# Kernel tuning notes

Hardware: AMD Instinct MI355X
Metric: run time of the kernel (lower is better)

Reference implementation:

```python
import jax, jax.numpy as jnp
import numpy as np

B, TQ, TK, D, R, H = 4, 2048, 2048, 1024, 64, 512
TAU_BASE, ASTRO_DECAY = 1.0, 0.95


def setup_inputs() -> dict:
    key = jax.random.key(0)
    ks = jax.random.split(key, 20)
    xav = lambda k, din, dout: jax.random.uniform(k, (din, dout), jnp.float32, -1.0, 1.0) * np.sqrt(6.0 / (din + dout))
    inp = {
        'q_in': jax.random.normal(ks[0], (B, TQ, D), jnp.float32),
        'k_in': jax.random.normal(ks[1], (B, TK, D), jnp.float32),
        'v_in': jax.random.normal(ks[2], (B, TK, D), jnp.float32),
        'astrocyte_state': jnp.zeros((B,), jnp.float32),
        'Wq': xav(ks[3], D, D), 'bq': jnp.zeros((D,), jnp.float32),
        'Wk': xav(ks[4], D, D), 'bk': jnp.zeros((D,), jnp.float32),
        'Wv': xav(ks[5], D, D), 'bv': jnp.zeros((D,), jnp.float32),
        'Wo': xav(ks[6], D, D), 'bo': jnp.zeros((D,), jnp.float32),
        # orthonormal role rows (R <= D): QR of a random D x R matrix, rows = Q^T
        'role_matrix': jnp.linalg.qr(jax.random.normal(ks[7], (D, R), jnp.float32))[0].T,
        'Wr1': xav(ks[8], D, H), 'br1': jnp.zeros((H,), jnp.float32),
        'Wr2': xav(ks[9], H, R),
        'astro_scale': jnp.ones((1,), jnp.float32),
    }
    return inp


def _l2norm(x, axis=-1, eps=1e-12):
    return x / jnp.clip(jnp.linalg.norm(x, axis=axis, keepdims=True), eps)


def _bind_vectors(a, b):
    # holographic (circular-convolution) binding via FFT along feature dim
    n = a.shape[-1]
    return jnp.fft.irfft(jnp.fft.rfft(a, axis=-1) * jnp.fft.rfft(b, axis=-1), n=n, axis=-1)


def _compute_surprise(Q):
    # per-token surprise: RMS-normalized L2 magnitude of projected queries -> (B, T_q)
    return jnp.linalg.norm(Q, axis=-1) / np.sqrt(Q.shape[-1])


def reference(q_in, k_in, v_in, astrocyte_state, Wq, bq, Wk, bk, Wv, bv, Wo, bo,
              role_matrix, Wr1, br1, Wr2, astro_scale):
    Q = q_in @ Wq + bq                      # (B,TQ,D)
    K = k_in @ Wk + bk                      # (B,TK,D)
    V = v_in @ Wv + bv                      # (B,TK,D)

    role_mat_norm = _l2norm(role_matrix)    # (R,D)
    role_logits = jax.nn.relu(K @ Wr1 + br1) @ Wr2          # (B,TK,R)
    role_weights = jax.nn.softmax(role_logits, axis=-1)
    role_vecs = role_weights @ role_mat_norm                 # (B,TK,D)
    K_bound = _bind_vectors(K, role_vecs)                    # (B,TK,D)

    surprise = _compute_surprise(Q)                          # (B,TQ)
    mean_surprise = surprise.mean(axis=-1)                   # (B,)
    new_state = ASTRO_DECAY * astrocyte_state + (1.0 - ASTRO_DECAY) * mean_surprise
    tau_eff = TAU_BASE * jnp.clip(1.0 + astro_scale * new_state, 0.001)[:, None, None]

    q_n = _l2norm(Q)
    k_n = _l2norm(K_bound)
    cos_sim = jnp.einsum('bqd,bkd->bqk', q_n, k_n)           # (B,TQ,TK)
    x = (cos_sim + 1.0) * 0.5
    scores = jnp.clip(1.0 - tau_eff * (1.0 - x) ** 2, 0.0)   # Epanechnikov kernel
    attn = scores / jnp.clip(scores.sum(axis=-1, keepdims=True), 1e-9)
    context = jnp.einsum('bqk,bkd->bqd', attn, V)
    output = context @ Wo + bo
    return output, new_state
```

## Files before the change

kernel.cpp:

```cpp
#include <hip/hip_runtime.h>
#include <stdint.h>


#define Bq 4
#define Tq 2048
#define Dd 1024
#define NT 8192
#define Hh 512
#define Rr_ 64
#define FQ 1024

typedef unsigned short ushort_t;
typedef short s16x8 __attribute__((ext_vector_type(8)));
typedef float floatx4 __attribute__((ext_vector_type(4)));

__device__ __forceinline__ float b2f(ushort_t s) {
  unsigned u = (unsigned)s << 16;
  return __builtin_bit_cast(float, u);
}
__device__ __forceinline__ ushort_t f2b(float f) {
  unsigned u = __builtin_bit_cast(unsigned, f);
  unsigned r = (u + 0x7fffu + ((u >> 16) & 1u)) >> 16;
  return (ushort_t)r;
}

__device__ __forceinline__ void load_lds16(const void* g, void* l) {
  __builtin_amdgcn_global_load_lds((__attribute__((address_space(1))) void*)(g),
                                   (__attribute__((address_space(3))) void*)(l),
                                   16, 0, 0);
}

__global__ __launch_bounds__(512, 2) void gemm256(
    const ushort_t* __restrict__ A, const ushort_t* __restrict__ Bt,
    float* __restrict__ C, ushort_t* __restrict__ Cbf,
    const float* __restrict__ bias_col, const float* __restrict__ bias_row,
    const float* __restrict__ rmul, int rmulStride,
    const float* __restrict__ cmul, int cmulStride,
    const float* __restrict__ tau,
    float* __restrict__ rowsum, int rsStride, int rsMode,
    int K, int lda, int ldb, int ldc,
    long long sA, long long sB, long long sC, int flags)
{
  __shared__ __align__(16) ushort_t lds[2][2][2][256][32];

  const int bz   = blockIdx.z;
  const ushort_t* Ab = A + (size_t)bz * sA;
  const ushort_t* Bb = Bt + (size_t)bz * sB;
  const int tm   = blockIdx.y * 256;
  const int tn   = blockIdx.x * 256;
  const int tid  = threadIdx.x;
  const int wave = tid >> 6;
  const int lane = tid & 63;
  const int wm   = wave >> 2;
  const int wn   = wave & 3;

  const int s_r  = lane >> 2;
  const int s_cg = (((lane & 3) - (s_r >> 1)) & 3);
  const int f_r  = lane & 15;
  const int f_p  = ((((lane >> 4) + (f_r >> 1)) & 3) << 3);

  const int NTILES = K >> 6;

  floatx4 acc[8][4] = {};

#define STAGE256(tt, g, sl)                                                     \
  do {                                                                          \
    const int mat_ = (g) & 1, h_ = (g) >> 1;                                    \
    const ushort_t* src_ = mat_ ? Bb : Ab;                                      \
    const int ld_ = mat_ ? ldb : lda;                                           \
    const int tb_ = mat_ ? tn : tm;                                             \
    const int kofs_ = (tt) * 64 + h_ * 32 + s_cg * 8;                           \
    _Pragma("unroll")                                                           \
    for (int j_ = 0; j_ < 2; j_++) {                                            \
      const int slab_ = wave * 2 + j_;                                          \
      const ushort_t* gp_ = src_ + (size_t)(tb_ + slab_ * 16 + s_r) * ld_ + kofs_; \
      load_lds16(gp_, (void*)&lds[sl][mat_][h_][slab_ * 16][0]);                \
    }                                                                           \
  } while (0)

  STAGE256(0, 0, 0);
  STAGE256(0, 1, 0);
  STAGE256(0, 2, 0);
  STAGE256(0, 3, 0);
  asm volatile("s_waitcnt vmcnt(4)" ::: "memory");
  __builtin_amdgcn_s_barrier();

  for (int t = 0; t < NTILES; t++) {
    const int sl  = t & 1;
    const int sl1 = sl ^ 1;
    const int tnx = (t + 1 < NTILES) ? t + 1 : t;
    s16x8 a[8], b[4];

#pragma unroll
    for (int m = 0; m < 8; m++)
      a[m] = *(const s16x8*)&lds[sl][0][0][wm * 128 + m * 16 + f_r][f_p];
#pragma unroll
    for (int n = 0; n < 4; n++)
      b[n] = *(const s16x8*)&lds[sl][1][0][wn * 64 + n * 16 + f_r][f_p];
    STAGE256(tnx, 0, sl1);
    __builtin_amdgcn_s_setprio(1);
#pragma unroll
    for (int m = 0; m < 8; m++)
#pragma unroll
      for (int n = 0; n < 2; n++)
        acc[m][n] = __builtin_amdgcn_mfma_f32_16x16x32_bf16(a[m], b[n], acc[m][n], 0, 0, 0);
    __builtin_amdgcn_s_setprio(0);
    __builtin_amdgcn_s_barrier();

    STAGE256(tnx, 1, sl1);
    __builtin_amdgcn_s_setprio(1);
#pragma unroll
    for (int m = 0; m < 8; m++)
#pragma unroll
      for (int n = 2; n < 4; n++)
        acc[m][n] = __builtin_amdgcn_mfma_f32_16x16x32_bf16(a[m], b[n], acc[m][n], 0, 0, 0);
    __builtin_amdgcn_s_setprio(0);
    asm volatile("s_waitcnt vmcnt(4)" ::: "memory");
    __builtin_amdgcn_s_barrier();

#pragma unroll
    for (int m = 0; m < 8; m++)
      a[m] = *(const s16x8*)&lds[sl][0][1][wm * 128 + m * 16 + f_r][f_p];
#pragma unroll
    for (int n = 0; n < 4; n++)
      b[n] = *(const s16x8*)&lds[sl][1][1][wn * 64 + n * 16 + f_r][f_p];
    STAGE256(tnx, 2, sl1);
    __builtin_amdgcn_s_setprio(1);
#pragma unroll
    for (int m = 0; m < 8; m++)
#pragma unroll
      for (int n = 0; n < 2; n++)
        acc[m][n] = __builtin_amdgcn_mfma_f32_16x16x32_bf16(a[m], b[n], acc[m][n], 0, 0, 0);
    __builtin_amdgcn_s_setprio(0);
    __builtin_amdgcn_s_barrier();

    STAGE256(tnx, 3, sl1);
    __builtin_amdgcn_s_setprio(1);
#pragma unroll
    for (int m = 0; m < 8; m++)
#pragma unroll
      for (int n = 2; n < 4; n++)
        acc[m][n] = __builtin_amdgcn_mfma_f32_16x16x32_bf16(a[m], b[n], acc[m][n], 0, 0, 0);
    __builtin_amdgcn_s_setprio(0);
    asm volatile("s_waitcnt vmcnt(4)" ::: "memory");
    __builtin_amdgcn_s_barrier();
  }
#undef STAGE256

  const float tv = tau ? tau[bz] : 0.f;
  float*   Cp  = C   ? C   + (size_t)bz * sC : nullptr;
  ushort_t* Cb = Cbf ? Cbf + (size_t)bz * sC : nullptr;
  float bcv[4], cmv[4];
#pragma unroll
  for (int n = 0; n < 4; n++) {
    const int col = tn + wn * 64 + n * 16 + (lane & 15);
    bcv[n] = bias_col ? bias_col[col] : 0.f;
    cmv[n] = cmul ? cmul[(size_t)bz * cmulStride + col] : 1.f;
  }
#pragma unroll
  for (int m = 0; m < 8; m++) {
#pragma unroll
    for (int r = 0; r < 4; r++) {
      const int row = tm + wm * 128 + m * 16 + (lane >> 4) * 4 + r;
      const float rm = rmul ? rmul[(size_t)bz * rmulStride + row] : 1.f;
      const float br = bias_row ? bias_row[row] : 0.f;
      float rsum = 0.f;
#pragma unroll
      for (int n = 0; n < 4; n++) {
        const int col = tn + wn * 64 + n * 16 + (lane & 15);
        float v;
        if (flags & 2) {
          v = acc[m][n][r] * (rm * cmv[n]) + bcv[n] + br;
        } else {
          v = (acc[m][n][r] + bcv[n] + br) * (rm * cmv[n]);
        }
        if (flags & 1) v = fmaxf(v, 0.f);
        if (tau) { float d = 1.0f - v; v = fmaxf(1.0f - tv * 0.25f * d * d, 0.f); }
        rsum += (rsMode == 2) ? v * v : v;
        if (Cp) Cp[(size_t)row * ldc + col] = v;
        if (Cb) Cb[(size_t)row * ldc + col] = f2b(v);
      }
      if (rsMode == 1 || rsMode == 2) {
        rsum += __shfl_xor(rsum, 1);
        rsum += __shfl_xor(rsum, 2);
        rsum += __shfl_xor(rsum, 4);
        rsum += __shfl_xor(rsum, 8);
        if ((lane & 15) == 0)
          atomicAdd(&rowsum[(size_t)bz * rsStride + row], rsum);
      }
    }
  }
}

__global__ __launch_bounds__(256) void gemm_bt(
    const ushort_t* __restrict__ A, const ushort_t* __restrict__ Bt,
    float* __restrict__ C, ushort_t* __restrict__ Cbf,
    const float* __restrict__ bias_col, const float* __restrict__ bias_row,
    const float* __restrict__ rmul, int rmulStride,
    const float* __restrict__ cmul, int cmulStride,
    const float* __restrict__ tau,
    float* __restrict__ rowsum, int rsStride, int rsMode,
    int K, int lda, int ldb, int ldc,
    long long sA, long long sB, long long sC, int flags)
{
  __shared__ __align__(16) ushort_t As[128 * 32];
  __shared__ __align__(16) ushort_t Bs[128 * 32];

  const int bz   = blockIdx.z;
  const ushort_t* Ab = A + (size_t)bz * sA;
  const ushort_t* Bb = Bt + (size_t)bz * sB;
  const int tm   = blockIdx.y * 128;
  const int tn   = blockIdx.x * 128;
  const int tid  = threadIdx.x;
  const int wave = tid >> 6;
  const int lane = tid & 63;
  const int wm   = (wave & 1) << 6;
  const int wn   = (wave >> 1) << 6;
  const int sr   = lane >> 2;
  const int cp   = lane & 3;
  const int sc   = (((cp - (sr >> 1)) & 3) << 3);
  const int fr   = lane & 15;
  const int fk   = ((((lane >> 4) + (fr >> 1)) & 3) << 3);

  floatx4 acc[4][4] = {};

  for (int k0 = 0; k0 < K; k0 += 32) {
    {
      const ushort_t* gA0 = Ab + (size_t)(tm + wave * 16 + sr) * lda + (k0 + sc);
      const ushort_t* gA1 = gA0 + (size_t)64 * lda;
      char* lA = (char*)As + wave * 1024;
      load_lds16(gA0, lA);
      load_lds16(gA1, lA + 4096);
      const ushort_t* gB0 = Bb + (size_t)(tn + wave * 16 + sr) * ldb + (k0 + sc);
      const ushort_t* gB1 = gB0 + (size_t)64 * ldb;
      char* lB = (char*)Bs + wave * 1024;
      load_lds16(gB0, lB);
      load_lds16(gB1, lB + 4096);
    }
    __syncthreads();
    s16x8 af[4], bfv[4];
#pragma unroll
    for (int i = 0; i < 4; i++)
      af[i] = *(const s16x8*)&As[(wm + i * 16 + fr) * 32 + fk];
#pragma unroll
    for (int j = 0; j < 4; j++)
      bfv[j] = *(const s16x8*)&Bs[(wn + j * 16 + fr) * 32 + fk];
#pragma unroll
    for (int i = 0; i < 4; i++)
#pragma unroll
      for (int j = 0; j < 4; j++)
        acc[i][j] = __builtin_amdgcn_mfma_f32_16x16x32_bf16(af[i], bfv[j], acc[i][j], 0, 0, 0);
    __syncthreads();
  }

  const float tv = tau ? tau[bz] : 0.f;
  float*   Cp  = C   ? C   + (size_t)bz * sC : nullptr;
  ushort_t* Cb = Cbf ? Cbf + (size_t)bz * sC : nullptr;
  float bcv[4], cmv[4];
#pragma unroll
  for (int j = 0; j < 4; j++) {
    const int col = tn + wn + j * 16 + (lane & 15);
    bcv[j] = bias_col ? bias_col[col] : 0.f;
    cmv[j] = cmul ? cmul[(size_t)bz * cmulStride + col] : 1.f;
  }
#pragma unroll
  for (int i = 0; i < 4; i++) {
#pragma unroll
    for (int r = 0; r < 4; r++) {
      const int row = tm + wm + i * 16 + (lane >> 4) * 4 + r;
      const float rm = rmul ? rmul[(size_t)bz * rmulStride + row] : 1.f;
      const float br = bias_row ? bias_row[row] : 0.f;
      float rsum = 0.f;
#pragma unroll
      for (int j = 0; j < 4; j++) {
        const int col = tn + wn + j * 16 + (lane & 15);
        float v;
        if (flags & 2) {
          v = acc[i][j][r] * (rm * cmv[j]) + bcv[j] + br;
        } else {
          v = (acc[i][j][r] + bcv[j] + br) * (rm * cmv[j]);
        }
        if (flags & 1) v = fmaxf(v, 0.f);
        if (tau) { float d = 1.0f - v; v = fmaxf(1.0f - tv * 0.25f * d * d, 0.f); }
        rsum += (rsMode == 2) ? v * v : v;
        if (Cp) Cp[(size_t)row * ldc + col] = v;
        if (Cb) Cb[(size_t)row * ldc + col] = f2b(v);
      }
      if (rsMode == 1 || rsMode == 2) {
        rsum += __shfl_xor(rsum, 1);
        rsum += __shfl_xor(rsum, 2);
        rsum += __shfl_xor(rsum, 4);
        rsum += __shfl_xor(rsum, 8);
        if ((lane & 15) == 0)
          atomicAdd(&rowsum[(size_t)bz * rsStride + row], rsum);
      }
    }
  }
}

struct P3 { const ushort_t* A[3]; const ushort_t* Bt[3]; ushort_t* C[3]; int M[3]; };

__global__ __launch_bounds__(256) void prep3(P3 p) {
  __shared__ __align__(16) ushort_t As[128 * 32];
  __shared__ __align__(16) ushort_t Bs[128 * 32];
  const int z  = blockIdx.z;
  const int tm = blockIdx.y * 128;
  if (tm >= p.M[z]) return;
  const ushort_t* Ab = p.A[z];
  const ushort_t* Bb = p.Bt[z];
  ushort_t*       Cc = p.C[z];
  const int tn   = blockIdx.x * 128;
  const int tid  = threadIdx.x;
  const int wave = tid >> 6;
  const int lane = tid & 63;
  const int wm   = (wave & 1) << 6;
  const int wn   = (wave >> 1) << 6;
  const int sr   = lane >> 2;
  const int cp   = lane & 3;
  const int sc   = (((cp - (sr >> 1)) & 3) << 3);
  const int fr   = lane & 15;
  const int fk   = ((((lane >> 4) + (fr >> 1)) & 3) << 3);

  floatx4 acc[4][4] = {};

  for (int k0 = 0; k0 < Dd; k0 += 32) {
    {
      const ushort_t* gA0 = Ab + (size_t)(tm + wave * 16 + sr) * Dd + (k0 + sc);
      const ushort_t* gA1 = gA0 + (size_t)64 * Dd;
      char* lA = (char*)As + wave * 1024;
      load_lds16(gA0, lA);
      load_lds16(gA1, lA + 4096);
      const ushort_t* gB0 = Bb + (size_t)(tn + wave * 16 + sr) * Dd + (k0 + sc);
      const ushort_t* gB1 = gB0 + (size_t)64 * Dd;
      char* lB = (char*)Bs + wave * 1024;
      load_lds16(gB0, lB);
      load_lds16(gB1, lB + 4096);
    }
    __syncthreads();
    s16x8 af[4], bfv[4];
#pragma unroll
    for (int i = 0; i < 4; i++)
      af[i] = *(const s16x8*)&As[(wm + i * 16 + fr) * 32 + fk];
#pragma unroll
    for (int j = 0; j < 4; j++)
      bfv[j] = *(const s16x8*)&Bs[(wn + j * 16 + fr) * 32 + fk];
#pragma unroll
    for (int i = 0; i < 4; i++)
#pragma unroll
      for (int j = 0; j < 4; j++)
        acc[i][j] = __builtin_amdgcn_mfma_f32_16x16x32_bf16(af[i], bfv[j], acc[i][j], 0, 0, 0);
    __syncthreads();
  }

#pragma unroll
  for (int i = 0; i < 4; i++)
#pragma unroll
    for (int r = 0; r < 4; r++) {
      const int row = tm + wm + i * 16 + (lane >> 4) * 4 + r;
#pragma unroll
      for (int j = 0; j < 4; j++) {
        const int col = tn + wn + j * 16 + (lane & 15);
        Cc[(size_t)row * Dd + col] = f2b(acc[i][j][r]);
      }
    }
}

__global__ __launch_bounds__(256) void castbf(const float* __restrict__ in,
                                              ushort_t* __restrict__ out, int n4) {
  int i = blockIdx.x * 256 + threadIdx.x;
  if (i >= n4) return;
  float4 v = ((const float4*)in)[i];
  ushort4 o;
  o.x = f2b(v.x); o.y = f2b(v.y); o.z = f2b(v.z); o.w = f2b(v.w);
  ((ushort4*)out)[i] = o;
}

struct TC4 { const float* in[4]; ushort_t* out[4]; };
__global__ __launch_bounds__(256) void tcast4(TC4 p) {
  __shared__ float t[32][33];
  int z = blockIdx.z;
  const float* in = p.in[z];
  ushort_t* out = p.out[z];
  int r0 = blockIdx.x * 32, c0 = blockIdx.y * 32;
  int x = threadIdx.x, y = threadIdx.y;
  for (int dy = 0; dy < 32; dy += 8)
    t[y + dy][x] = in[(size_t)(r0 + y + dy) * 1024 + c0 + x];
  __syncthreads();
  for (int dy = 0; dy < 32; dy += 8)
    out[(size_t)(c0 + y + dy) * 1024 + r0 + x] = f2b(t[x][y + dy]);
}

__global__ __launch_bounds__(256) void tcast(const float* __restrict__ in,
                                             ushort_t* __restrict__ out,
                                             int RrN, int Cc, int Cp) {
  __shared__ float t[32][33];
  int r0 = blockIdx.x * 32, c0 = blockIdx.y * 32;
  int x = threadIdx.x, y = threadIdx.y;
  for (int dy = 0; dy < 32; dy += 8) {
    int r = r0 + y + dy, c = c0 + x;
    t[y + dy][x] = (c < Cc) ? in[(size_t)r * Cc + c] : 0.f;
  }
  __syncthreads();
  for (int dy = 0; dy < 32; dy += 8) {
    int c = c0 + y + dy, r = r0 + x;
    if (c < Cp) out[(size_t)c * RrN + r] = f2b(t[x][y + dy]);
  }
}

__global__ __launch_bounds__(256) void rolenorm(const float* __restrict__ rm,
                                                ushort_t* __restrict__ rmn) {
  int r = blockIdx.x, tid = threadIdx.x;
  float4 v = ((const float4*)(rm + (size_t)r * 1024))[tid];
  float s = v.x * v.x + v.y * v.y + v.z * v.z + v.w * v.w;
#pragma unroll
  for (int m = 1; m < 64; m <<= 1) s += __shfl_xor(s, m);
  __shared__ float red[6];
  if ((tid & 63) == 0) red[tid >> 6] = s;
  __syncthreads();
  if (tid == 0) red[4] = 1.f / fmaxf(sqrtf(red[0] + red[1] + red[2] + red[3]), 1e-12f);
  __syncthreads();
  float inv = red[4];
  ushort4 o;
  o.x = f2b(v.x * inv); o.y = f2b(v.y * inv); o.z = f2b(v.z * inv); o.w = f2b(v.w * inv);
  ((ushort4*)(rmn + (size_t)r * 1024))[tid] = o;
}

__global__ __launch_bounds__(256) void rfn_kernel(const ushort_t* __restrict__ rmn,
                                                  const ushort_t* __restrict__ ftab,
                                                  ushort_t* __restrict__ RFnT) {
  int f = blockIdx.x;
  int t = threadIdx.x;
  int r = t >> 2, part = t & 3;
  const ushort_t* fr = ftab + (size_t)f * 1024 + part * 256;
  const ushort_t* rr = rmn + (size_t)r * 1024 + part * 256;
  float s = 0.f;
#pragma unroll 4
  for (int i = 0; i < 32; i++) {
    s16x8 a = *(const s16x8*)(fr + i * 8);
    s16x8 b = *(const s16x8*)(rr + i * 8);
#pragma unroll
    for (int j = 0; j < 8; j++) s += b2f((ushort_t)a[j]) * b2f((ushort_t)b[j]);
  }
  s += __shfl_xor(s, 1);
  s += __shfl_xor(s, 2);
  if (part == 0) RFnT[(size_t)f * 128 + r] = f2b(s);
}

__global__ __launch_bounds__(64) void foldbk(const ushort_t* __restrict__ ftab,
                                             const float* __restrict__ bk,
                                             float* __restrict__ bkF) {
  int j = blockIdx.x, lane = threadIdx.x;
  const ushort_t* row = ftab + (size_t)j * 1024 + lane * 16;
  const float* bp = bk + lane * 16;
  float s = 0.f;
#pragma unroll
  for (int i = 0; i < 2; i++) {
    s16x8 a = *(const s16x8*)(row + i * 8);
#pragma unroll
    for (int e = 0; e < 8; e++) s += b2f((ushort_t)a[e]) * bp[i * 8 + e];
  }
#pragma unroll
  for (int m = 1; m < 64; m <<= 1) s += __shfl_xor(s, m);
  if (lane == 0) bkF[j] = s;
}

__global__ __launch_bounds__(256) void foldbh(const float* __restrict__ Wr1,
                                              const float* __restrict__ bk,
                                              const float* __restrict__ br1,
                                              float* __restrict__ bh) {
  int h = blockIdx.x * 256 + threadIdx.x;
  float s = br1[h];
  for (int d = 0; d < 1024; d++) s += bk[d] * Wr1[(size_t)d * Hh + h];
  bh[h] = s;
}

__global__ __launch_bounds__(256) void foldbvo(const float* __restrict__ Wo,
                                               const float* __restrict__ bv,
                                               const float* __restrict__ bo,
                                               float* __restrict__ bvo) {
  int d = blockIdx.x * 256 + threadIdx.x;
  float s = bo[d];
  for (int e = 0; e < 1024; e++) s += bv[e] * Wo[(size_t)e * 1024 + d];
  bvo[d] = s;
}

__global__ __launch_bounds__(256) void invnorm_surprise(const float* __restrict__ ssq,
                                                        float* __restrict__ invn,
                                                        float* __restrict__ ssum) {
  int row = blockIdx.x * 256 + threadIdx.x;
  float nrm = sqrtf(ssq[row]);
  invn[row] = 1.f / fmaxf(nrm, 1e-12f);
  float t = nrm;
#pragma unroll
  for (int m = 1; m < 64; m <<= 1) t += __shfl_xor(t, m);
  if ((threadIdx.x & 63) == 0) atomicAdd(&ssum[row >> 11], t);
}

__global__ __launch_bounds__(256) void invnorm(const float* __restrict__ ssq,
                                               float* __restrict__ invn) {
  int row = blockIdx.x * 256 + threadIdx.x;
  invn[row] = 1.f / fmaxf(sqrtf(ssq[row]), 1e-12f);
}

__global__ __launch_bounds__(256) void invrowsum(const float* __restrict__ rs,
                                                 float* __restrict__ inv) {
  int row = blockIdx.x * 256 + threadIdx.x;
  inv[row] = 1.f / fmaxf(rs[row], 1e-9f);
}

__global__ void finalize_astro(const float* __restrict__ ssum, const float* __restrict__ astro,
                               const float* __restrict__ ascale, float* __restrict__ tau,
                               float* __restrict__ outTail) {
  int b = threadIdx.x;
  if (b < Bq) {
    float mean = ssum[b] * (1.f / (32.f * 2048.f));
    float ns = 0.95f * astro[b] + 0.05f * mean;
    tau[b] = fmaxf(1.f + ascale[0] * ns, 0.001f);
    outTail[b] = ns;
  }
}

__global__ __launch_bounds__(256) void softmax64(const float* __restrict__ logits,
                                                 ushort_t* __restrict__ out) {
  int row = blockIdx.x * 4 + (threadIdx.x >> 6);
  int lane = threadIdx.x & 63;
  float x = logits[(size_t)row * 128 + lane];
  float m = x;
#pragma unroll
  for (int s = 1; s < 64; s <<= 1) m = fmaxf(m, __shfl_xor(m, s));
  float e = expf(x - m);
  float sum = e;
#pragma unroll
  for (int s = 1; s < 64; s <<= 1) sum += __shfl_xor(sum, s);
  out[(size_t)row * 64 + lane] = f2b(e / sum);
}

__global__ __launch_bounds__(256) void gen_ftab(ushort_t* __restrict__ ftab) {
  const float TW = 6.283185307179586f / 1024.f;
  int idx = blockIdx.x * 256 + threadIdx.x;
  int j = idx >> 10, k = idx & 1023;
  int f = j <= 512 ? j : j - 512;
  float th = (float)((f * k) & 1023) * TW;
  float sv, cv; sincosf(th, &sv, &cv);
  ftab[idx] = f2b(j <= 512 ? cv : -sv);
}

__global__ __launch_bounds__(256) void gen_itab(ushort_t* __restrict__ itab) {
  const float TW = 6.283185307179586f / 1024.f;
  int idx = blockIdx.x * 256 + threadIdx.x;
  int n = idx >> 10, j = idx & 1023;
  float v;
  if (j <= 512) {
    float w = (j == 0 || j == 512) ? (1.f / 1024.f) : (2.f / 1024.f);
    float th = (float)((j * n) & 1023) * TW;
    float sv, cv; sincosf(th, &sv, &cv);
    v = w * cv;
  } else {
    int f = j - 512;
    float th = (float)((f * n) & 1023) * TW;
    float sv, cv; sincosf(th, &sv, &cv);
    v = -(2.f / 1024.f) * sv;
  }
  itab[idx] = f2b(v);
}

__global__ __launch_bounds__(256) void fftmul(const ushort_t* __restrict__ KF,
                                              const ushort_t* __restrict__ RF,
                                              ushort_t* __restrict__ P) {
  int idx = blockIdx.x * 256 + threadIdx.x;
  int t = idx >> 9;
  int j = idx & 511;
  size_t base = (size_t)t * FQ;
  if (j == 0) {
    P[base]       = f2b(b2f(KF[base]) * b2f(RF[base]));
    P[base + 512] = f2b(b2f(KF[base + 512]) * b2f(RF[base + 512]));
  } else {
    float a = b2f(KF[base + j]), b = b2f(KF[base + 512 + j]);
    float c = b2f(RF[base + j]), d = b2f(RF[base + 512 + j]);
    P[base + j]       = f2b(a * c - b * d);
    P[base + 512 + j] = f2b(a * d + b * c);
  }
}

static constexpr size_t OFF_RS    = 0;
static constexpr size_t OFF_SSQQ  = 32768;
static constexpr size_t OFF_SSQK  = 65536;
static constexpr size_t OFF_INVQ  = 98304;
static constexpr size_t OFF_INVK  = 131072;
static constexpr size_t OFF_INVRS = 163840;
static constexpr size_t OFF_SSUM  = 196608;
static constexpr size_t OFF_TAU   = 196864;
static constexpr size_t OFF_WQT   = 197120;
static constexpr size_t OFF_WKB   = OFF_WQT  + 2097152;
static constexpr size_t OFF_WVB   = OFF_WKB  + 2097152;
static constexpr size_t OFF_WOT   = OFF_WVB  + 2097152;
static constexpr size_t OFF_WR1T  = OFF_WOT  + 2097152;
static constexpr size_t OFF_WR2T  = OFF_WR1T + 1048576;
static constexpr size_t OFF_RMN   = OFF_WR2T + 131072;
static constexpr size_t OFF_FTAB  = OFF_RMN  + 131072;
static constexpr size_t OFF_ITAB  = OFF_FTAB + 2097152;
static constexpr size_t OFF_RFNT  = OFF_ITAB + 2097152;
static constexpr size_t OFF_B1    = OFF_RFNT + 262144;
static constexpr size_t OFF_B2    = OFF_B1   + 16777216;
static constexpr size_t OFF_B3    = OFF_B2   + 16777216;
static constexpr size_t OFF_B4    = OFF_B3   + 16777216;
static constexpr size_t OFF_B5    = OFF_B4   + 16777216;
static constexpr size_t OFF_B6    = OFF_B5   + 16777216;
static constexpr size_t OFF_B7    = OFF_B6   + 16777216;
static constexpr size_t OFF_HID   = OFF_B7   + 16777216;
static constexpr size_t OFF_LOGI  = OFF_HID  + 8388608;
static constexpr size_t OFF_RW    = OFF_LOGI + 4194304;
static constexpr size_t OFF_SB    = OFF_RW   + 1048576;
static constexpr size_t WS_NEEDED = OFF_SB   + 33554432;
static constexpr size_t OFF_WKF   = OFF_B6;
static constexpr size_t OFF_WOV   = OFF_B6 + 2097152;
static constexpr size_t OFF_WKR1  = OFF_B6 + 4194304;
static constexpr size_t OFF_BKF   = OFF_B6 + 5242880;
static constexpr size_t OFF_BH    = OFF_B6 + 5247232;
static constexpr size_t OFF_BVO   = OFF_B6 + 5249536;

static inline void launch_gemm(hipStream_t s, const ushort_t* A, const ushort_t* Bt,
                               float* Cf, ushort_t* Cb,
                               const float* bias_col, const float* bias_row,
                               const float* rmul, int rmulStride,
                               const float* cmul, int cmulStride,
                               const float* tau, float* rowsum, int rsStride, int rsMode,
                               int M, int N, int K, int lda, int ldb, int ldc,
                               long long sA, long long sB, long long sC, int Z, int flags) {
  dim3 g(N / 128, M / 128, Z), b(256);
  gemm_bt<<<g, b, 0, s>>>(A, Bt, Cf, Cb, bias_col, bias_row, rmul, rmulStride,
                          cmul, cmulStride, tau, rowsum, rsStride, rsMode,
                          K, lda, ldb, ldc, sA, sB, sC, flags);
}

static inline void launch_gemm256(hipStream_t s, const ushort_t* A, const ushort_t* Bt,
                                  float* Cf, ushort_t* Cb,
                                  const float* bias_col, const float* bias_row,
                                  const float* rmul, int rmulStride,
                                  const float* cmul, int cmulStride,
                                  const float* tau, float* rowsum, int rsStride, int rsMode,
                                  int M, int N, int K, int lda, int ldb, int ldc,
                                  long long sA, long long sB, long long sC, int Z, int flags) {
  dim3 g(N / 256, M / 256, Z), b(512);
  gemm256<<<g, b, 0, s>>>(A, Bt, Cf, Cb, bias_col, bias_row, rmul, rmulStride,
                          cmul, cmulStride, tau, rowsum, rsStride, rsMode,
                          K, lda, ldb, ldc, sA, sB, sC, flags);
}

extern "C" void kernel_launch(void* const* d_in, const int* in_sizes, int n_in,
                              void* d_out, int out_size, void* d_ws, size_t ws_size,
                              hipStream_t stream) {
  (void)in_sizes; (void)n_in; (void)out_size;
  if (ws_size < WS_NEEDED) return;

  const float* q_in  = (const float*)d_in[0];
  const float* k_in  = (const float*)d_in[1];
  const float* v_in  = (const float*)d_in[2];
  const float* astro = (const float*)d_in[3];
  const float* Wq    = (const float*)d_in[4];
  const float* bq    = (const float*)d_in[5];
  const float* Wk    = (const float*)d_in[6];
  const float* bk    = (const float*)d_in[7];
  const float* Wv    = (const float*)d_in[8];
  const float* bv    = (const float*)d_in[9];
  const float* Wo    = (const float*)d_in[10];
  const float* bo    = (const float*)d_in[11];
  const float* roleM = (const float*)d_in[12];
  const float* Wr1   = (const float*)d_in[13];
  const float* br1   = (const float*)d_in[14];
  const float* Wr2   = (const float*)d_in[15];
  const float* ascl  = (const float*)d_in[16];

  char* ws = (char*)d_ws;
  float*    rowsumS = (float*)(ws + OFF_RS);
  float*    ssqQ    = (float*)(ws + OFF_SSQQ);
  float*    ssqK    = (float*)(ws + OFF_SSQK);
  float*    invQ    = (float*)(ws + OFF_INVQ);
  float*    invK    = (float*)(ws + OFF_INVK);
  float*    invRS   = (float*)(ws + OFF_INVRS);
  float*    ssum    = (float*)(ws + OFF_SSUM);
  float*    tau     = (float*)(ws + OFF_TAU);
  ushort_t* WqT  = (ushort_t*)(ws + OFF_WQT);
  ushort_t* Wkb  = (ushort_t*)(ws + OFF_WKB);
  ushort_t* Wvb  = (ushort_t*)(ws + OFF_WVB);
  ushort_t* WoT  = (ushort_t*)(ws + OFF_WOT);
  ushort_t* Wr1T = (ushort_t*)(ws + OFF_WR1T);
  ushort_t* Wr2T = (ushort_t*)(ws + OFF_WR2T);
  ushort_t* rmn  = (ushort_t*)(ws + OFF_RMN);
  ushort_t* FTab = (ushort_t*)(ws + OFF_FTAB);
  ushort_t* ITab = (ushort_t*)(ws + OFF_ITAB);
  ushort_t* RFnT = (ushort_t*)(ws + OFF_RFNT);
  ushort_t* qbf  = (ushort_t*)(ws + OFF_B1);
  ushort_t* KF   = (ushort_t*)(ws + OFF_B1);
  ushort_t* kinb = (ushort_t*)(ws + OFF_B2);
  ushort_t* RF   = (ushort_t*)(ws + OFF_B2);
  ushort_t* vinb = (ushort_t*)(ws + OFF_B3);
  ushort_t* Pb   = (ushort_t*)(ws + OFF_B3);
  ushort_t* qraw = (ushort_t*)(ws + OFF_B4);
  ushort_t* kbraw= (ushort_t*)(ws + OFF_B5);
  ushort_t* WkF  = (ushort_t*)(ws + OFF_WKF);
  ushort_t* Wov  = (ushort_t*)(ws + OFF_WOV);
  ushort_t* WkR1 = (ushort_t*)(ws + OFF_WKR1);
  float*    bkF  = (float*)(ws + OFF_BKF);
  float*    bh   = (float*)(ws + OFF_BH);
  float*    bvo  = (float*)(ws + OFF_BVO);
  ushort_t* vT   = (ushort_t*)(ws + OFF_B7);
  ushort_t* hid  = (ushort_t*)(ws + OFF_HID);
  float*    logi = (float*)(ws + OFF_LOGI);
  ushort_t* rw   = (ushort_t*)(ws + OFF_RW);
  ushort_t* Sb   = (ushort_t*)(ws + OFF_SB);
  float*    out  = (float*)d_out;

  hipMemsetAsync(ws, 0, OFF_SSUM + 256, stream);

  TC4 tc4;
  tc4.in[0] = Wq; tc4.out[0] = WqT;
  tc4.in[1] = Wo; tc4.out[1] = WoT;
  tc4.in[2] = Wq; tc4.out[2] = WqT;
  tc4.in[3] = Wq; tc4.out[3] = WqT;
  tcast4<<<dim3(32, 32, 2), dim3(32, 8), 0, stream>>>(tc4);
  castbf<<<1024, 256, 0, stream>>>(Wk, Wkb, 262144);
  castbf<<<1024, 256, 0, stream>>>(Wv, Wvb, 262144);
  tcast<<<dim3(32, 16), dim3(32, 8), 0, stream>>>(Wr1, Wr1T, 1024, 512, 512);
  tcast<<<dim3(16, 4),  dim3(32, 8), 0, stream>>>(Wr2, Wr2T, 512, 64, 128);
  rolenorm<<<64, 256, 0, stream>>>(roleM, rmn);
  gen_ftab<<<(FQ * 1024) / 256, 256, 0, stream>>>(FTab);
  gen_itab<<<(1024 * FQ) / 256, 256, 0, stream>>>(ITab);
  rfn_kernel<<<FQ, 256, 0, stream>>>(rmn, FTab, RFnT);

  P3 p3;
  p3.A[0] = FTab; p3.Bt[0] = Wkb; p3.C[0] = WkF;  p3.M[0] = 1024;
  p3.A[1] = WoT;  p3.Bt[1] = Wvb; p3.C[1] = Wov;  p3.M[1] = 1024;
  p3.A[2] = Wr1T; p3.Bt[2] = Wkb; p3.C[2] = WkR1; p3.M[2] = 512;
  prep3<<<dim3(8, 8, 3), 256, 0, stream>>>(p3);
  foldbk<<<1024, 64, 0, stream>>>(FTab, bk, bkF);
  foldbh<<<Hh / 256, 256, 0, stream>>>(Wr1, bk, br1, bh);
  foldbvo<<<Dd / 256, 256, 0, stream>>>(Wo, bv, bo, bvo);

  castbf<<<8192, 256, 0, stream>>>(q_in, qbf, NT * Dd / 4);
  launch_gemm256(stream, qbf, WqT, nullptr, qraw, bq, nullptr,
                 nullptr, 0, nullptr, 0, nullptr, ssqQ, 0, 2,
                 NT, Dd, Dd, Dd, Dd, Dd, 0, 0, 0, 1, 0);
  invnorm_surprise<<<NT / 256, 256, 0, stream>>>(ssqQ, invQ, ssum);
  finalize_astro<<<1, 64, 0, stream>>>(ssum, astro, ascl, tau, out + (size_t)NT * Dd);

  castbf<<<8192, 256, 0, stream>>>(k_in, kinb, NT * Dd / 4);
  launch_gemm(stream, kinb, WkR1, nullptr, hid, bh, nullptr,
              nullptr, 0, nullptr, 0, nullptr, nullptr, 0, 0,
              NT, Hh, Dd, Dd, Dd, Hh, 0, 0, 0, 1, 1 );
  launch_gemm(stream, hid, Wr2T, logi, nullptr, nullptr, nullptr,
              nullptr, 0, nullptr, 0, nullptr, nullptr, 0, 0,
              NT, 128, Hh, Hh, Hh, 128, 0, 0, 0, 1, 0);
  softmax64<<<NT / 4, 256, 0, stream>>>(logi, rw);

  launch_gemm256(stream, kinb, WkF, nullptr, KF, bkF, nullptr,
                 nullptr, 0, nullptr, 0, nullptr, nullptr, 0, 0,
                 NT, FQ, Dd, Dd, Dd, FQ, 0, 0, 0, 1, 0);
  launch_gemm(stream, rw, RFnT, nullptr, RF, nullptr, nullptr,
              nullptr, 0, nullptr, 0, nullptr, nullptr, 0, 0,
              NT, FQ, Rr_, Rr_, 128, FQ, 0, 0, 0, 1, 0);

  castbf<<<8192, 256, 0, stream>>>(v_in, vinb, NT * Dd / 4);
  launch_gemm256(stream, Wov, vinb, nullptr, vT, nullptr, nullptr,
                 nullptr, 0, nullptr, 0, nullptr, nullptr, 0, 0,
                 Dd, NT, Dd, Dd, Dd, NT, 0, 0, 0, 1, 0);

  fftmul<<<(NT * 512) / 256, 256, 0, stream>>>(KF, RF, Pb);
  launch_gemm256(stream, Pb, ITab, nullptr, kbraw, nullptr, nullptr,
                 nullptr, 0, nullptr, 0, nullptr, ssqK, 0, 2,
                 NT, Dd, FQ, FQ, FQ, Dd, 0, 0, 0, 1, 0);
  invnorm<<<NT / 256, 256, 0, stream>>>(ssqK, invK);

  launch_gemm256(stream, qraw, kbraw, nullptr, Sb, nullptr, nullptr,
                 invQ, Tq, invK, Tq, tau, rowsumS, Tq, 1,
                 Tq, Tq, Dd, Dd, Dd, Tq,
                 (long long)Tq * Dd, (long long)Tq * Dd, (long long)Tq * Tq, Bq, 0);
  invrowsum<<<NT / 256, 256, 0, stream>>>(rowsumS, invRS);
  launch_gemm256(stream, Sb, vT, out, nullptr, bvo, nullptr,
                 invRS, Tq, nullptr, 0, nullptr, nullptr, 0, 0,
                 Tq, Dd, Tq, Tq, NT, Dd,
                 (long long)Tq * Tq, (long long)Tq, (long long)Tq * Dd, Bq, 2 );
}
```

Measured before the change: 791.2 us.

## Deepen GEMM prefetch pipeline and add XCD-aware block swizzling

The 256-tile GEMM now prefetches half of the tile two steps ahead into the slot currently being consumed, so loads are issued further in advance of the MFMA work that needs them. The mid-iteration vmcnt wait is removed and barriers are added after each stage issue. Both GEMM kernels also remap block indices so consecutive logical tiles land on the same XCD, which should improve L2 reuse. The extra barriers add synchronisation cost, and the tighter slot reuse depends on correct ordering of outstanding loads.

```diff
diff --git a/kernel.cpp b/kernel.cpp
--- a/kernel.cpp
+++ b/kernel.cpp
@@ -28,6 +28,19 @@
   __builtin_amdgcn_global_load_lds((__attribute__((address_space(1))) void*)(g),
                                    (__attribute__((address_space(3))) void*)(l),
                                    16, 0, 0);
+}
+
+__device__ __forceinline__ void xcd_swizzle(int& bx, int& by, int& bz) {
+  const int gx = gridDim.x, gy = gridDim.y, gz = gridDim.z;
+  const int nwg = gx * gy * gz;
+  const int orig = (bz * gy + by) * gx + bx;
+  const int q = nwg >> 3, r = nwg & 7;
+  const int x = orig & 7, i = orig >> 3;
+  const int wg = (x < r ? x * (q + 1) : r * (q + 1) + (x - r) * q) + i;
+  bx = wg % gx;
+  const int t = wg / gx;
+  by = t % gy;
+  bz = t / gy;
 }
 
 __global__ __launch_bounds__(512, 2) void gemm256(
@@ -43,11 +56,12 @@
 {
   __shared__ __align__(16) ushort_t lds[2][2][2][256][32];
 
-  const int bz   = blockIdx.z;
+  int bx = blockIdx.x, by = blockIdx.y, bz = blockIdx.z;
+  xcd_swizzle(bx, by, bz);
   const ushort_t* Ab = A + (size_t)bz * sA;
   const ushort_t* Bb = Bt + (size_t)bz * sB;
-  const int tm   = blockIdx.y * 256;
-  const int tn   = blockIdx.x * 256;
+  const int tm   = by * 256;
+  const int tn   = bx * 256;
   const int tid  = threadIdx.x;
   const int wave = tid >> 6;
   const int lane = tid & 63;
@@ -82,13 +96,16 @@
   STAGE256(0, 1, 0);
   STAGE256(0, 2, 0);
   STAGE256(0, 3, 0);
+  STAGE256(1, 0, 1);
+  STAGE256(1, 1, 1);
   asm volatile("s_waitcnt vmcnt(4)" ::: "memory");
   __builtin_amdgcn_s_barrier();
 
   for (int t = 0; t < NTILES; t++) {
     const int sl  = t & 1;
     const int sl1 = sl ^ 1;
-    const int tnx = (t + 1 < NTILES) ? t + 1 : t;
+    const int t1  = (t + 1 < NTILES) ? t + 1 : t;
+    const int t2  = (t + 2 < NTILES) ? t + 2 : t;
     s16x8 a[8], b[4];
 
 #pragma unroll
@@ -97,7 +114,8 @@
 #pragma unroll
     for (int n = 0; n < 4; n++)
       b[n] = *(const s16x8*)&lds[sl][1][0][wn * 64 + n * 16 + f_r][f_p];
-    STAGE256(tnx, 0, sl1);
+    STAGE256(t1, 2, sl1);
+    __builtin_amdgcn_s_barrier();
     __builtin_amdgcn_s_setprio(1);
 #pragma unroll
     for (int m = 0; m < 8; m++)
@@ -107,7 +125,8 @@
     __builtin_amdgcn_s_setprio(0);
     __builtin_amdgcn_s_barrier();
 
-    STAGE256(tnx, 1, sl1);
+    STAGE256(t1, 3, sl1);
+    __builtin_amdgcn_s_barrier();
     __builtin_amdgcn_s_setprio(1);
 #pragma unroll
     for (int m = 0; m < 8; m++)
@@ -115,7 +134,6 @@
       for (int n = 2; n < 4; n++)
         acc[m][n] = __builtin_amdgcn_mfma_f32_16x16x32_bf16(a[m], b[n], acc[m][n], 0, 0, 0);
     __builtin_amdgcn_s_setprio(0);
-    asm volatile("s_waitcnt vmcnt(4)" ::: "memory");
     __builtin_amdgcn_s_barrier();
 
 #pragma unroll
@@ -124,7 +142,8 @@
 #pragma unroll
     for (int n = 0; n < 4; n++)
       b[n] = *(const s16x8*)&lds[sl][1][1][wn * 64 + n * 16 + f_r][f_p];
-    STAGE256(tnx, 2, sl1);
+    STAGE256(t2, 0, sl);
+    __builtin_amdgcn_s_barrier();
     __builtin_amdgcn_s_setprio(1);
 #pragma unroll
     for (int m = 0; m < 8; m++)
@@ -134,7 +153,8 @@
     __builtin_amdgcn_s_setprio(0);
     __builtin_amdgcn_s_barrier();
 
-    STAGE256(tnx, 3, sl1);
+    STAGE256(t2, 1, sl);
+    __builtin_amdgcn_s_barrier();
     __builtin_amdgcn_s_setprio(1);
 #pragma unroll
     for (int m = 0; m < 8; m++)
@@ -206,11 +226,12 @@
   __shared__ __align__(16) ushort_t As[128 * 32];
   __shared__ __align__(16) ushort_t Bs[128 * 32];
 
-  const int bz   = blockIdx.z;
+  int bx = blockIdx.x, by = blockIdx.y, bz = blockIdx.z;
+  xcd_swizzle(bx, by, bz);
   const ushort_t* Ab = A + (size_t)bz * sA;
   const ushort_t* Bb = Bt + (size_t)bz * sB;
-  const int tm   = blockIdx.y * 128;
-  const int tn   = blockIdx.x * 128;
+  const int tm   = by * 128;
+  const int tn   = bx * 128;
   const int tid  = threadIdx.x;
   const int wave = tid >> 6;
   const int lane = tid & 63;
```

Result: no change. 804.5 us (+1.7%).
